# Kernel optimization log

Measured on AMD Instinct MI355X. Metric: run time of the kernel, lower is better.

## Reference

```python
import jax, jax.numpy as jnp
import numpy as np

NEG_SLOPE = 0.2

def _gc(inp, adj, W, b):
    # Kipf GraphConvolution: adj @ (inp @ W) + b
    return adj @ (inp @ W) + b

def _lrelu(x):
    return jnp.where(x >= 0, x, NEG_SLOPE * x)

def setup_inputs() -> dict:
    key = jax.random.key(0)
    ks = jax.random.split(key, 24)
    Nx, Ny, Fx, Fy, D1, C = 8192, 4096, 512, 256, 256, 64
    s = 0.05
    inp = {
        "hx1": jax.random.uniform(ks[0], (Nx, Nx), jnp.float32) / Nx,
        "hx2": jax.random.uniform(ks[1], (Nx, Ny), jnp.float32) / Ny,
        "x0": jax.random.normal(ks[2], (Nx, Fx), jnp.float32),
        "hy1": jax.random.uniform(ks[3], (Ny, Ny), jnp.float32) / Ny,
        "hy2": jax.random.uniform(ks[4], (Ny, Nx), jnp.float32) / Nx,
        "y0": jax.random.normal(ks[5], (Ny, Fy), jnp.float32),
        "alpha": jnp.float32(0.6),
        "beta": jnp.float32(0.4),
        # weights/biases of the 8 GraphConvolution layers
        "Wx1a": jax.random.normal(ks[6], (Fx, D1), jnp.float32) * s,
        "bx1a": jnp.zeros((D1,), jnp.float32),
        "Wx1b": jax.random.normal(ks[7], (Fy, D1), jnp.float32) * s,
        "bx1b": jnp.zeros((D1,), jnp.float32),
        "Wx2a": jax.random.normal(ks[8], (D1, C), jnp.float32) * s,
        "bx2a": jnp.zeros((C,), jnp.float32),
        "Wx2b": jax.random.normal(ks[9], (D1, C), jnp.float32) * s,
        "bx2b": jnp.zeros((C,), jnp.float32),
        "Wy1a": jax.random.normal(ks[10], (Fy, D1), jnp.float32) * s,
        "by1a": jnp.zeros((D1,), jnp.float32),
        "Wy1b": jax.random.normal(ks[11], (Fx, D1), jnp.float32) * s,
        "by1b": jnp.zeros((D1,), jnp.float32),
        "Wy2a": jax.random.normal(ks[12], (D1, C), jnp.float32) * s,
        "by2a": jnp.zeros((C,), jnp.float32),
        "Wy2b": jax.random.normal(ks[13], (D1, C), jnp.float32) * s,
        "by2b": jnp.zeros((C,), jnp.float32),
    }
    return inp

def reference(hx1, hx2, x0, hy1, hy2, y0, alpha, beta,
              Wx1a, bx1a, Wx1b, bx1b, Wx2a, bx2a, Wx2b, bx2b,
              Wy1a, by1a, Wy1b, by1b, Wy2a, by2a, Wy2b, by2b):
    # layer 1
    x1 = _lrelu(_gc(x0, hx1, Wx1a, bx1a) * alpha + _gc(y0, hx2, Wx1b, bx1b) * (1 - alpha))
    y1 = _lrelu(_gc(y0, hy1, Wy1a, by1a) * beta + _gc(x0, hy2, Wy1b, by1b) * (1 - beta))
    # layer 2
    x2 = _lrelu(_gc(x1, hx1, Wx2a, bx2a) * alpha + _gc(y1, hx2, Wx2b, bx2b) * (1 - alpha))
    y_pre = _gc(y1, hy1, Wy2a, by2a) * beta + _gc(x1, hy2, Wy2b, by2b) * (1 - beta)
    y2 = _lrelu(y_pre)
    h_hat = jax.nn.sigmoid(x2 @ y2.T)            # [Nx, Ny]
    x_output = jax.nn.log_softmax(x2, axis=1)    # [Nx, nclass]
    return (h_hat, x_output)
```

## Files before the change

kernel.cpp:

```cpp
#include <hip/hip_runtime.h>

typedef unsigned short u16;
typedef unsigned char u8;
typedef long i64;
typedef __attribute__((ext_vector_type(8))) short bf16x8;
typedef __attribute__((ext_vector_type(4))) float f32x4;
typedef __attribute__((ext_vector_type(8))) u16 u16x8;
typedef __attribute__((ext_vector_type(4))) u16 u16x4;
typedef __attribute__((ext_vector_type(4))) float f4;

#define DEVI static __device__ __forceinline__

DEVI u16 f2b(float f) { __bf16 h = (__bf16)f; return __builtin_bit_cast(u16, h); }
DEVI float b2f(u16 h) { unsigned u = ((unsigned)h) << 16; return __builtin_bit_cast(float, u); }

DEVI int pk8(float a, float b, float c, float d) {
  int w = __builtin_amdgcn_cvt_pk_fp8_f32(a, b, 0, false);
  return __builtin_amdgcn_cvt_pk_fp8_f32(c, d, w, true);
}

DEVI void gload16(const void* g, void* l) {
  __builtin_amdgcn_global_load_lds((const __attribute__((address_space(1))) void*)g,
                                   (__attribute__((address_space(3))) void*)l, 16, 0, 0);
}

__global__ __launch_bounds__(1024)
void gemmF_k(const float* __restrict__ A0, const float* __restrict__ A1,
             const u8* __restrict__ B0, const u8* __restrict__ B1,
             u8* __restrict__ A0f8, u8* __restrict__ A1f8,
             int K0, int K1, int L0, int L1,
             u16* __restrict__ Cout, size_t MN)
{
  constexpr int BM = 128, BK = 64;
  constexpr int LDA = 72;
  constexpr int ASZ = BM * LDA;
  constexpr int BSZ = 256 * BK;
  constexpr int BUFSZ = ASZ + BSZ;
  constexpr float SADJ = 8192.f;
  __shared__ __align__(16) u8 lds[4 * BUFSZ];

  const int tid = threadIdx.x, lane = tid & 63, wave = tid >> 6;
  const int wm = (wave >> 2) * 32, wn = (wave & 3) * 64;
  const int lgrp = lane >> 4, lrow = lane & 15;

  const int gy = gridDim.y;
  const int flat = blockIdx.y + gy * blockIdx.z;
  const int nwg = gy * gridDim.z;
  const int swz = (flat & 7) * (nwg >> 3) + (flat >> 3);
  const int m0 = (swz % gy) * BM;
  const int z  = swz / gy;

  const int nt0 = L0 >> 6, NT = nt0 + (L1 >> 6);

  const int r0 = tid >> 4;
  const int cf = (tid & 15) << 2;

  f32x4 acc[2][4];
#pragma unroll
  for (int m = 0; m < 2; ++m)
#pragma unroll
    for (int n = 0; n < 4; ++n) acc[m][n] = (f32x4){0.f, 0.f, 0.f, 0.f};

  f4 rA0[2], rA1[2];

  auto tileinfo = [&](int t, const float*& Ap, const u8*& Bp, u8*& Af8, int& Kj, int& kk) {
    if (t < nt0) { Ap = A0; Bp = B0; Af8 = A0f8; Kj = K0; kk = z * L0 + (t << 6); }
    else         { Ap = A1; Bp = B1; Af8 = A1f8; Kj = K1; kk = z * L1 + ((t - nt0) << 6); }
  };

  auto loadA = [&](int t, f4 (&r)[2]) {
    const float* Ap; const u8* Bp; u8* Af8; int Kj, kk;
    tileinfo(t, Ap, Bp, Af8, Kj, kk);
#pragma unroll
    for (int j = 0; j < 2; ++j) {
      const int rr = j * 64 + r0;
      r[j] = __builtin_nontemporal_load(
          (const f4*)(Ap + (size_t)(m0 + rr) * Kj + kk + cf));
    }
  };

  auto loadB = [&](int t) {
    const float* Ap; const u8* Bp; u8* Af8; int Kj, kk;
    tileinfo(t, Ap, Bp, Af8, Kj, kk);
    u8* sB = &lds[(t & 3) * BUFSZ] + ASZ;
    const int off = tid * 16;
    const int r = off >> 6, c = off & 63;
    gload16(Bp + (size_t)r * Kj + kk + (c ^ (((r >> 1) & 3) << 4)), sB + off);
  };

  auto writeA = [&](int t, f4 (&r)[2]) {
    const float* Ap; const u8* Bp; u8* Af8; int Kj, kk;
    tileinfo(t, Ap, Bp, Af8, Kj, kk);
    u8* sA = &lds[(t & 3) * BUFSZ];
#pragma unroll
    for (int j = 0; j < 2; ++j) {
      const int rr = j * 64 + r0;
      const int pw = pk8(r[j][0] * SADJ, r[j][1] * SADJ, r[j][2] * SADJ, r[j][3] * SADJ);
      *(int*)&sA[rr * LDA + cf] = pw;
      *(int*)(Af8 + (size_t)(m0 + rr) * Kj + kk + cf) = pw;
    }
  };

  auto compute = [&](int t) {
    const u8* sA = &lds[(t & 3) * BUFSZ];
    const u8* sB = sA + ASZ;
    __builtin_amdgcn_s_setprio(1);
#pragma unroll
    for (int ks = 0; ks < 2; ++ks) {
      i64 a[2], b[4];
#pragma unroll
      for (int m = 0; m < 2; ++m) {
        const int r = wm + m * 16 + lrow;
        a[m] = *(const i64*)&sA[r * LDA + ks * 32 + lgrp * 8];
      }
#pragma unroll
      for (int n = 0; n < 4; ++n) {
        const int r = wn + n * 16 + lrow;
        b[n] = *(const i64*)&sB[r * BK + ((ks * 32 + lgrp * 8) ^ (((r >> 1) & 3) << 4))];
      }
#pragma unroll
      for (int m = 0; m < 2; ++m)
#pragma unroll
        for (int n = 0; n < 4; ++n)
          acc[m][n] = __builtin_amdgcn_mfma_f32_16x16x32_fp8_fp8(a[m], b[n], acc[m][n], 0, 0, 0);
    }
    __builtin_amdgcn_s_setprio(0);
  };

  auto step = [&](int t, f4 (&rIn)[2], f4 (&rOut)[2]) {
    const bool has_next = (t + 1 < NT);
    if (has_next) { loadA(t + 1, rOut); loadB(t + 1); }
    if (!has_next)   asm volatile("s_waitcnt vmcnt(0)" ::: "memory");
    else if (t == 0) asm volatile("s_waitcnt vmcnt(3)" ::: "memory");
    else             asm volatile("s_waitcnt vmcnt(5)" ::: "memory");
    writeA(t, rIn);
    asm volatile("s_waitcnt lgkmcnt(0)" ::: "memory");
    asm volatile("s_barrier" ::: "memory");
    compute(t);
  };

  loadA(0, rA0); loadB(0);

  for (int t = 0; t < NT; t += 2) {
    step(t, rA0, rA1);
    step(t + 1, rA1, rA0);
  }

  u16* Cp = Cout + (size_t)z * MN;
#pragma unroll
  for (int n = 0; n < 4; ++n) {
    const int c = wn + n * 16 + lrow;
#pragma unroll
    for (int m = 0; m < 2; ++m) {
      const int rb = m0 + wm + m * 16 + lgrp * 4;
#pragma unroll
      for (int q = 0; q < 4; ++q)
        Cp[(size_t)(rb + q) * 256 + c] = f2b(acc[m][n][q]);
    }
  }
}

__global__ __launch_bounds__(256)
void gemm8_k(const u8* __restrict__ xA0, const u8* __restrict__ xA1,
             const u8* __restrict__ xB0, const u8* __restrict__ xB1,
             int xK0, int xK1, int xL0, int xL1, u16* __restrict__ xC, size_t xMN,
             const u8* __restrict__ yA0, const u8* __restrict__ yA1,
             const u8* __restrict__ yB0, const u8* __restrict__ yB1,
             int yK0, int yK1, int yL0, int yL1, u16* __restrict__ yC, size_t yMN)
{
  constexpr int BM = 128, BK = 128, BN = 64;
  constexpr int MR = 4, NR = 2;
  constexpr int ASZ = BM * BK, BSZ = BN * BK;
  __shared__ __align__(16) u8 lds[3 * (ASZ + BSZ)];

  const int tid = threadIdx.x, lane = tid & 63, wave = tid >> 6;
  const int wm = (wave >> 1) * 64, wn = (wave & 1) * 32;
  const int lgrp = lane >> 4, lrow = lane & 15;

  const int flat = blockIdx.x;
  const int nwg = gridDim.x;
  const int swz = (flat & 7) * (nwg >> 3) + (flat >> 3);

  const u8 *A0, *A1, *B0, *B1; int K0, K1, L0, L1; u16* Cw; size_t MN;
  int m0, z;
  if (swz < 512) {
    A0=xA0; A1=xA1; B0=xB0; B1=xB1; K0=xK0; K1=xK1; L0=xL0; L1=xL1; Cw=xC; MN=xMN;
    m0 = (swz & 63) * BM; z = swz >> 6;
  } else {
    const int id = swz - 512;
    A0=yA0; A1=yA1; B0=yB0; B1=yB1; K0=yK0; K1=yK1; L0=yL0; L1=yL1; Cw=yC; MN=yMN;
    m0 = (id & 31) * BM; z = id >> 5;
  }

  const int nt0 = L0 >> 7, NT = nt0 + (L1 >> 7);

  f32x4 acc[MR][NR];
#pragma unroll
  for (int m = 0; m < MR; ++m)
#pragma unroll
    for (int n = 0; n < NR; ++n) acc[m][n] = (f32x4){0.f, 0.f, 0.f, 0.f};

  auto stage = [&](int buf, int t) {
    const u8* Ap; const u8* Bp; int Kj, kk;
    if (t < nt0) { Ap = A0; Bp = B0; Kj = K0; kk = z * L0 + (t << 7); }
    else         { Ap = A1; Bp = B1; Kj = K1; kk = z * L1 + ((t - nt0) << 7); }
    u8* sA = &lds[buf * (ASZ + BSZ)];
    u8* sB = sA + ASZ;
#pragma unroll
    for (int i = 0; i < ASZ / 4096; ++i) {
      const int off = i * 4096 + tid * 16;
      const int r = off >> 7, c = off & 127;
      gload16(Ap + (size_t)(m0 + r) * Kj + kk + (c ^ ((r & 7) << 4)), sA + off);
    }
#pragma unroll
    for (int i = 0; i < BSZ / 4096; ++i) {
      const int off = i * 4096 + tid * 16;
      const int r = off >> 7, c = off & 127;
      gload16(Bp + (size_t)r * Kj + kk + (c ^ ((r & 7) << 4)), sB + off);
    }
  };

  auto compute = [&](int buf) {
    const u8* sA = &lds[buf * (ASZ + BSZ)];
    const u8* sB = sA + ASZ;
    __builtin_amdgcn_s_setprio(1);
#pragma unroll
    for (int ks = 0; ks < 4; ++ks) {
      i64 a[MR], b[NR];
#pragma unroll
      for (int m = 0; m < MR; ++m) {
        const int r = wm + m * 16 + lrow;
        a[m] = *(const i64*)&sA[r * BK + ((ks * 32 + lgrp * 8) ^ ((r & 7) << 4))];
      }
#pragma unroll
      for (int n = 0; n < NR; ++n) {
        const int r = wn + n * 16 + lrow;
        b[n] = *(const i64*)&sB[r * BK + ((ks * 32 + lgrp * 8) ^ ((r & 7) << 4))];
      }
#pragma unroll
      for (int m = 0; m < MR; ++m)
#pragma unroll
        for (int n = 0; n < NR; ++n)
          acc[m][n] = __builtin_amdgcn_mfma_f32_16x16x32_fp8_fp8(a[m], b[n], acc[m][n], 0, 0, 0);
    }
    __builtin_amdgcn_s_setprio(0);
  };

  stage(0, 0);
  stage(1, 1);
  for (int t = 0; t < NT; ++t) {
    if (t + 1 < NT) asm volatile("s_waitcnt vmcnt(6)" ::: "memory");
    else            asm volatile("s_waitcnt vmcnt(0)" ::: "memory");
    asm volatile("s_barrier" ::: "memory");
    compute(t % 3);
    if (t + 2 < NT) stage((t + 2) % 3, t + 2);
  }

  u16* Cp = Cw + (size_t)z * MN;
#pragma unroll
  for (int n = 0; n < NR; ++n) {
    const int c = wn + n * 16 + lrow;
#pragma unroll
    for (int m = 0; m < MR; ++m) {
      const int rb = m0 + wm + m * 16 + lgrp * 4;
#pragma unroll
      for (int q = 0; q < 4; ++q)
        Cp[(size_t)(rb + q) * 64 + c] = f2b(acc[m][n][q]);
    }
  }
}

template<bool A_F32>
__global__ __launch_bounds__(256)
void gemmS_k(const void* Ax, const u16* Bx, int Kx, int ldcx, u8* Cx1, u8* Cx2,
             const void* Ay, const u16* By, int Ky, int ldcy, u8* Cy1, u8* Cy2,
             int ySplit, int nsplit, float sOut)
{
  constexpr int BM = 64, BN = 64, BK = 32, LD = 40;
  constexpr int MR = 2, NR = 2;
  __shared__ u16 sA[BM * LD];
  __shared__ u16 sB[BN * LD];

  const int tid  = threadIdx.x;
  const int lane = tid & 63;
  const int wave = tid >> 6;
  const int wm = (wave >> 1) * 32;
  const int wn = (wave &  1) * 32;

  const void* A0_; const u16* B0_; int K0, ldc; u8 *C1, *C2; int m0;
  if ((int)blockIdx.y < ySplit) {
    A0_ = Ax; B0_ = Bx; K0 = Kx; ldc = ldcx; C1 = Cx1; C2 = Cx2;
    m0 = blockIdx.y * BM;
  } else {
    A0_ = Ay; B0_ = By; K0 = Ky; ldc = ldcy; C1 = Cy1; C2 = Cy2;
    m0 = (blockIdx.y - ySplit) * BM;
  }
  const int n0 = blockIdx.x * BN;

  constexpr int TPRA = 256 / BM;
  constexpr int EPTA = 32 / TPRA;
  const int ar = tid / TPRA, ac = (tid % TPRA) * EPTA;
  const int br = ar, bc = ac;

  f32x4 acc[MR][NR];
#pragma unroll
  for (int m = 0; m < MR; ++m)
#pragma unroll
    for (int n = 0; n < NR; ++n) acc[m][n] = (f32x4){0.f, 0.f, 0.f, 0.f};

  const int lgrp = lane >> 4, lrow = lane & 15;

  for (int kk = 0; kk < K0; kk += BK) {
    if constexpr (A_F32) {
      const float* Ap = (const float*)A0_ + (size_t)(m0 + ar) * K0 + kk + ac;
      f4 v0 = ((const f4*)Ap)[0];
      f4 v1 = ((const f4*)Ap)[1];
      u16x8 h;
      h[0]=f2b(v0[0]); h[1]=f2b(v0[1]); h[2]=f2b(v0[2]); h[3]=f2b(v0[3]);
      h[4]=f2b(v1[0]); h[5]=f2b(v1[1]); h[6]=f2b(v1[2]); h[7]=f2b(v1[3]);
      *(u16x8*)&sA[ar * LD + ac] = h;
    } else {
      const u16* Ap = (const u16*)A0_ + (size_t)(m0 + ar) * K0 + kk + ac;
      *(u16x8*)&sA[ar * LD + ac] = *(const u16x8*)Ap;
    }
    {
      const u16* Bp = B0_ + (size_t)(n0 + br) * K0 + kk + bc;
      *(u16x8*)&sB[br * LD + bc] = *(const u16x8*)Bp;
    }
    __syncthreads();
    bf16x8 af[MR], bfr[NR];
#pragma unroll
    for (int m = 0; m < MR; ++m)
      af[m] = *(const bf16x8*)&sA[(wm + m * 16 + lrow) * LD + lgrp * 8];
#pragma unroll
    for (int n = 0; n < NR; ++n)
      bfr[n] = *(const bf16x8*)&sB[(wn + n * 16 + lrow) * LD + lgrp * 8];
#pragma unroll
    for (int m = 0; m < MR; ++m)
#pragma unroll
      for (int n = 0; n < NR; ++n)
        acc[m][n] = __builtin_amdgcn_mfma_f32_16x16x32_bf16(af[m], bfr[n], acc[m][n], 0, 0, 0);
    __syncthreads();
  }

#pragma unroll
  for (int n = 0; n < NR; ++n) {
    const int c = n0 + wn + n * 16 + lrow;
    u8* Cp = (c < nsplit) ? C1 : C2;
    const int cr = (c < nsplit) ? c : c - nsplit;
#pragma unroll
    for (int m = 0; m < MR; ++m) {
      const int rb = m0 + wm + m * 16 + lgrp * 4;
      int w = __builtin_amdgcn_cvt_pk_fp8_f32(acc[m][n][0] * sOut, acc[m][n][1] * sOut, 0, false);
      w = __builtin_amdgcn_cvt_pk_fp8_f32(acc[m][n][2] * sOut, acc[m][n][3] * sOut, w, true);
      *(int*)&Cp[(size_t)cr * ldc + rb] = w;
    }
  }
}

__global__ __launch_bounds__(256)
void gemmH_k(const u16* A0_, const u16* B0_, int K0, float* Cout, int ldc)
{
  constexpr int BM = 128, BN = 128, BK = 32, LD = 40;
  constexpr int MR = 4, NR = 4;
  __shared__ u16 sA[BM * LD];
  __shared__ u16 sB[BN * LD];

  const int tid  = threadIdx.x;
  const int lane = tid & 63;
  const int wave = tid >> 6;
  const int wm = (wave >> 1) * 64;
  const int wn = (wave &  1) * 64;
  const int m0 = blockIdx.y * BM;
  const int n0 = blockIdx.x * BN;

  constexpr int TPRA = 2;
  constexpr int EPTA = 16;
  const int ar = tid / TPRA, ac = (tid % TPRA) * EPTA;

  f32x4 acc[MR][NR];
#pragma unroll
  for (int m = 0; m < MR; ++m)
#pragma unroll
    for (int n = 0; n < NR; ++n) acc[m][n] = (f32x4){0.f, 0.f, 0.f, 0.f};

  const int lgrp = lane >> 4, lrow = lane & 15;

  for (int kk = 0; kk < K0; kk += BK) {
    {
      const u16* Ap = A0_ + (size_t)(m0 + ar) * K0 + kk + ac;
      *(u16x8*)&sA[ar * LD + ac]     = ((const u16x8*)Ap)[0];
      *(u16x8*)&sA[ar * LD + ac + 8] = ((const u16x8*)Ap)[1];
      const u16* Bp = B0_ + (size_t)(n0 + ar) * K0 + kk + ac;
      *(u16x8*)&sB[ar * LD + ac]     = ((const u16x8*)Bp)[0];
      *(u16x8*)&sB[ar * LD + ac + 8] = ((const u16x8*)Bp)[1];
    }
    __syncthreads();
    bf16x8 af[MR], bfr[NR];
#pragma unroll
    for (int m = 0; m < MR; ++m)
      af[m] = *(const bf16x8*)&sA[(wm + m * 16 + lrow) * LD + lgrp * 8];
#pragma unroll
    for (int n = 0; n < NR; ++n)
      bfr[n] = *(const bf16x8*)&sB[(wn + n * 16 + lrow) * LD + lgrp * 8];
#pragma unroll
    for (int m = 0; m < MR; ++m)
#pragma unroll
      for (int n = 0; n < NR; ++n)
        acc[m][n] = __builtin_amdgcn_mfma_f32_16x16x32_bf16(af[m], bfr[n], acc[m][n], 0, 0, 0);
    __syncthreads();
  }

  float* Cp = Cout;
#pragma unroll
  for (int n = 0; n < NR; ++n) {
    const int c = n0 + wn + n * 16 + lrow;
#pragma unroll
    for (int m = 0; m < MR; ++m) {
      const int rb = m0 + wm + m * 16 + lgrp * 4;
#pragma unroll
      for (int q = 0; q < 4; ++q)
        Cp[(size_t)(rb + q) * ldc + c] = 1.f / (1.f + __expf(-acc[m][n][q]));
    }
  }
}

__global__ __launch_bounds__(256)
void combine_k(const u16* __restrict__ parts, int KS, int N, size_t MN,
               const float* b0, const float* b1, const float* mixp, u16* out, float invs)
{
  const float mix = *mixp;
  const size_t stride = (size_t)gridDim.x * 1024;
  for (size_t i = ((size_t)blockIdx.x * 256 + threadIdx.x) * 4; i < MN; i += stride) {
    f4 s = {0.f, 0.f, 0.f, 0.f};
    for (int zz = 0; zz < KS; ++zz) {
      u16x4 pv = *(const u16x4*)&parts[(size_t)zz * MN + i];
#pragma unroll
      for (int q = 0; q < 4; ++q) s[q] += b2f(pv[q]);
    }
    const int c = (int)(i % (size_t)N);
    u16x4 o;
#pragma unroll
    for (int q = 0; q < 4; ++q) {
      float v = s[q] * invs + mix * b0[c + q] + (1.f - mix) * b1[c + q];
      v = v >= 0.f ? v : 0.2f * v;
      o[q] = f2b(v);
    }
    *(u16x4*)&out[i] = o;
  }
}

__global__ __launch_bounds__(256)
void prep_w(const float* Wx1a, const float* Wx1b, const float* Wy1a, const float* Wy1b,
            const float* Wx2a, const float* Wx2b, const float* Wy2a, const float* Wy2b,
            u16* WtX, u16* WtY, u16* W2X, u16* W2Y,
            const float* ap, const float* bp)
{
  const int zz = blockIdx.z;
  const float a = *ap, b = *bp;
  const float* W; u16* O; int K, N, roff; float s;
  switch (zz) {
    case 0: W=Wx1a; O=WtX; K=512; N=256; roff=0;   s=a;      break;
    case 1: W=Wy1b; O=WtX; K=512; N=256; roff=256; s=1.f-b;  break;
    case 2: W=Wx1b; O=WtY; K=256; N=256; roff=0;   s=1.f-a;  break;
    case 3: W=Wy1a; O=WtY; K=256; N=256; roff=256; s=b;      break;
    case 4: W=Wx2a; O=W2X; K=256; N=64;  roff=0;   s=a;      break;
    case 5: W=Wy2b; O=W2X; K=256; N=64;  roff=64;  s=1.f-b;  break;
    case 6: W=Wx2b; O=W2Y; K=256; N=64;  roff=0;   s=1.f-a;  break;
    default:W=Wy2a; O=W2Y; K=256; N=64;  roff=64;  s=b;      break;
  }
  const int total = K * N;
  for (int i = blockIdx.x * 256 + threadIdx.x; i < total; i += gridDim.x * 256) {
    const int k = i / N, n = i - k * N;
    O[(size_t)(n + roff) * K + k] = f2b(W[i] * s);
  }
}

__global__ __launch_bounds__(256)
void softmax_k(const u16* x, float* out)
{
  const int row  = blockIdx.x * 4 + (threadIdx.x >> 6);
  const int lane = threadIdx.x & 63;
  const float v = b2f(x[row * 64 + lane]);
  float m = v;
#pragma unroll
  for (int off = 32; off; off >>= 1) m = fmaxf(m, __shfl_xor(m, off));
  float s = __expf(v - m);
#pragma unroll
  for (int off = 32; off; off >>= 1) s += __shfl_xor(s, off);
  out[(size_t)row * 64 + lane] = v - m - __logf(s);
}

extern "C" void kernel_launch(void* const* d_in, const int* in_sizes, int n_in,
                              void* d_out, int out_size, void* d_ws, size_t ws_size,
                              hipStream_t stream)
{
  const float* hx1 = (const float*)d_in[0];
  const float* hx2 = (const float*)d_in[1];
  const float* x0  = (const float*)d_in[2];
  const float* hy1 = (const float*)d_in[3];
  const float* hy2 = (const float*)d_in[4];
  const float* y0  = (const float*)d_in[5];
  const float* alphap = (const float*)d_in[6];
  const float* betap  = (const float*)d_in[7];
  const float* Wx1a = (const float*)d_in[8];  const float* bx1a = (const float*)d_in[9];
  const float* Wx1b = (const float*)d_in[10]; const float* bx1b = (const float*)d_in[11];
  const float* Wx2a = (const float*)d_in[12]; const float* bx2a = (const float*)d_in[13];
  const float* Wx2b = (const float*)d_in[14]; const float* bx2b = (const float*)d_in[15];
  const float* Wy1a = (const float*)d_in[16]; const float* by1a = (const float*)d_in[17];
  const float* Wy1b = (const float*)d_in[18]; const float* by1b = (const float*)d_in[19];
  const float* Wy2a = (const float*)d_in[20]; const float* by2a = (const float*)d_in[21];
  const float* Wy2b = (const float*)d_in[22]; const float* by2b = (const float*)d_in[23];
  (void)in_sizes; (void)n_in; (void)out_size;

  constexpr int Nx = 8192, Ny = 4096, Fx = 512, Fy = 256, D1 = 256, C = 64;
  constexpr float SB1 = 16.f, SB2 = 256.f;
  constexpr float INV1 = 1.f / (8192.f * 16.f);
  constexpr float INV2 = 1.f / (8192.f * 256.f);
  constexpr int KSx = 4, KSy = 8;

  u8* wsb = (u8*)d_ws;
  size_t off = 0;
  auto alloc = [&](size_t n) { u8* p = wsb + off; off += (n + 63) & ~(size_t)63; return p; };

  u16* WtX = (u16*)alloc((size_t)512 * 512 * 2);
  u16* WtY = (u16*)alloc((size_t)512 * 256 * 2);
  u16* W2X = (u16*)alloc((size_t)128 * 256 * 2);
  u16* W2Y = (u16*)alloc((size_t)128 * 256 * 2);
  u8* B1x  = alloc((size_t)D1 * Nx);
  u8* B2x  = alloc((size_t)D1 * Ny);
  u8* B1y  = alloc((size_t)D1 * Ny);
  u8* B2y  = alloc((size_t)D1 * Nx);
  u16* x1  = (u16*)alloc((size_t)Nx * D1 * 2);
  u16* y1  = (u16*)alloc((size_t)Ny * D1 * 2);
  u8* B1x2 = alloc((size_t)C * Nx);
  u8* B2x2 = alloc((size_t)C * Ny);
  u8* B1y2 = alloc((size_t)C * Ny);
  u8* B2y2 = alloc((size_t)C * Nx);
  u16* x2  = (u16*)alloc((size_t)Nx * C * 2);
  u16* y2  = (u16*)alloc((size_t)Ny * C * 2);

  const size_t base_off = off;
  const size_t szHx1 = (size_t)Nx * Nx, szHx2 = (size_t)Nx * Ny;
  const size_t szHy1 = (size_t)Ny * Ny, szHy2 = (size_t)Ny * Nx;
  const size_t needA = base_off + szHx1 + szHx2 + szHy1 + szHy2 + ((size_t)32 << 20) + (1 << 20);

  u8 *hx1f8, *hx2f8, *hy1f8, *hy2f8; u16* part;
  if (ws_size >= needA) {
    hx1f8 = alloc(szHx1); hx2f8 = alloc(szHx2);
    hy1f8 = alloc(szHy1); hy2f8 = alloc(szHy2);
    part  = (u16*)alloc((size_t)32 << 20);
  } else {
    hy1f8 = alloc(szHy1); hy2f8 = alloc(szHy2);
    hx1f8 = (u8*)d_out;
    hx2f8 = (u8*)d_out + szHx1;
    part  = (u16*)((u8*)d_out + szHx1 + szHx2);
  }

  const size_t MNx1 = (size_t)Nx * D1, MNy1 = (size_t)Ny * D1;
  const size_t MNx2 = (size_t)Nx * C,  MNy2 = (size_t)Ny * C;

  prep_w<<<dim3(256, 1, 8), 256, 0, stream>>>(Wx1a, Wx1b, Wy1a, Wy1b, Wx2a, Wx2b, Wy2a, Wy2b,
      WtX, WtY, W2X, W2Y, alphap, betap);

  gemmS_k<true><<<dim3(8, Nx/64 + Ny/64), 256, 0, stream>>>(
      x0, WtX, Fx, Nx, B1x, B2y,
      y0, WtY, Fy, Ny, B2x, B1y,
      Nx/64, 256, SB1);

  gemmF_k<<<dim3(1, Nx/128, KSx), 1024, 0, stream>>>(hx1, hx2, B1x, B2x, hx1f8, hx2f8,
      Nx, Ny, Nx/KSx, Ny/KSx, part, MNx1);
  combine_k<<<dim3(2048), 256, 0, stream>>>(part, KSx, D1, MNx1, bx1a, bx1b, alphap, x1, INV1);
  gemmF_k<<<dim3(1, Ny/128, KSy), 1024, 0, stream>>>(hy1, hy2, B1y, B2y, hy1f8, hy2f8,
      Ny, Nx, Ny/KSy, Nx/KSy, part, MNy1);
  combine_k<<<dim3(1024), 256, 0, stream>>>(part, KSy, D1, MNy1, by1a, by1b, betap, y1, INV1);

  gemmS_k<false><<<dim3(2, Nx/64 + Ny/64), 256, 0, stream>>>(
      x1, W2X, D1, Nx, B1x2, B2y2,
      y1, W2Y, D1, Ny, B2x2, B1y2,
      Nx/64, 64, SB2);

  u16* partY2 = part + 8 * MNx2;
  gemm8_k<<<dim3(1024), 256, 0, stream>>>(
      hx1f8, hx2f8, B1x2, B2x2, Nx, Ny, 1024, 512, part, MNx2,
      hy1f8, hy2f8, B1y2, B2y2, Ny, Nx, 256, 512, partY2, MNy2);
  combine_k<<<dim3(512), 256, 0, stream>>>(part, 8, C, MNx2, bx2a, bx2b, alphap, x2, INV2);
  combine_k<<<dim3(256), 256, 0, stream>>>(partY2, 16, C, MNy2, by2a, by2b, betap, y2, INV2);

  gemmH_k<<<dim3(Ny/128, Nx/128), 256, 0, stream>>>(x2, y2, C, (float*)d_out, Ny);

  softmax_k<<<dim3(Nx/4), 256, 0, stream>>>(x2, (float*)d_out + (size_t)Nx * Ny);
}
```

Before: 345.0 us.

## Merge x/y layer-1 GEMMs and combines into single launches, fuse softmax into combine

The two layer-1 fp32-adjacency GEMMs (x and y sides) now run as one 512-block launch that picks its operand set from the swizzled block id. The two layer-1 combines become one kernel, and the layer-2 combines are merged with the log-softmax so x2 is never re-read. The final sigmoid output uses nontemporal stores. This cuts launch count and tail effects and lets the two sides overlap. The cost is hardcoded grid splits (256 x blocks, KSx=4 assumed, column index & 255) that tie the code to these exact shapes.

After: 345.6 us. Within noise of the previous version (+0.2%).

```diff
diff --git a/kernel.cpp b/kernel.cpp
--- a/kernel.cpp
+++ b/kernel.cpp
@@ -25,11 +25,14 @@
 }
 
 __global__ __launch_bounds__(1024)
-void gemmF_k(const float* __restrict__ A0, const float* __restrict__ A1,
-             const u8* __restrict__ B0, const u8* __restrict__ B1,
-             u8* __restrict__ A0f8, u8* __restrict__ A1f8,
-             int K0, int K1, int L0, int L1,
-             u16* __restrict__ Cout, size_t MN)
+void gemmF_k(const float* __restrict__ xA0, const float* __restrict__ xA1,
+             const u8* __restrict__ xB0, const u8* __restrict__ xB1,
+             u8* __restrict__ xA0f8, u8* __restrict__ xA1f8,
+             int xK0, int xK1, int xL0, int xL1, u16* __restrict__ xC, size_t xMN,
+             const float* __restrict__ yA0, const float* __restrict__ yA1,
+             const u8* __restrict__ yB0, const u8* __restrict__ yB1,
+             u8* __restrict__ yA0f8, u8* __restrict__ yA1f8,
+             int yK0, int yK1, int yL0, int yL1, u16* __restrict__ yC, size_t yMN)
 {
   constexpr int BM = 128, BK = 64;
   constexpr int LDA = 72;
@@ -43,12 +46,22 @@
   const int wm = (wave >> 2) * 32, wn = (wave & 3) * 64;
   const int lgrp = lane >> 4, lrow = lane & 15;
 
-  const int gy = gridDim.y;
-  const int flat = blockIdx.y + gy * blockIdx.z;
-  const int nwg = gy * gridDim.z;
+  const int flat = blockIdx.x;
+  const int nwg = gridDim.x;
   const int swz = (flat & 7) * (nwg >> 3) + (flat >> 3);
-  const int m0 = (swz % gy) * BM;
-  const int z  = swz / gy;
+
+  const float *A0, *A1; const u8 *B0, *B1; u8 *A0f8, *A1f8;
+  int K0, K1, L0, L1; u16* Cout; size_t MN; int m0, z;
+  if (swz < 256) {
+    A0=xA0; A1=xA1; B0=xB0; B1=xB1; A0f8=xA0f8; A1f8=xA1f8;
+    K0=xK0; K1=xK1; L0=xL0; L1=xL1; Cout=xC; MN=xMN;
+    m0 = (swz & 63) * BM; z = swz >> 6;
+  } else {
+    const int id = swz - 256;
+    A0=yA0; A1=yA1; B0=yB0; B1=yB1; A0f8=yA0f8; A1f8=yA1f8;
+    K0=yK0; K1=yK1; L0=yL0; L1=yL1; Cout=yC; MN=yMN;
+    m0 = (id & 31) * BM; z = id >> 5;
+  }
 
   const int nt0 = L0 >> 6, NT = nt0 + (L1 >> 6);
 
@@ -420,25 +433,38 @@
       const int rb = m0 + wm + m * 16 + lgrp * 4;
 #pragma unroll
       for (int q = 0; q < 4; ++q)
-        Cp[(size_t)(rb + q) * ldc + c] = 1.f / (1.f + __expf(-acc[m][n][q]));
+        __builtin_nontemporal_store(1.f / (1.f + __expf(-acc[m][n][q])),
+                                    &Cp[(size_t)(rb + q) * ldc + c]);
     }
   }
 }
 
 __global__ __launch_bounds__(256)
-void combine_k(const u16* __restrict__ parts, int KS, int N, size_t MN,
-               const float* b0, const float* b1, const float* mixp, u16* out, float invs)
-{
+void combine1_k(const u16* __restrict__ partX, const u16* __restrict__ partY,
+                int xBlocks, size_t MNx, size_t MNy, int KSx_, int KSy_,
+                const float* bxa, const float* bxb, const float* ap,
+                const float* bya, const float* byb, const float* bp,
+                u16* x1, u16* y1, float invs)
+{
+  const u16* parts; size_t MN; int KS, nb, bid = blockIdx.x;
+  const float *b0, *b1, *mixp; u16* out;
+  if (bid < xBlocks) {
+    parts = partX; MN = MNx; KS = KSx_; b0 = bxa; b1 = bxb; mixp = ap; out = x1; nb = xBlocks;
+  } else {
+    bid -= xBlocks;
+    parts = partY; MN = MNy; KS = KSy_; b0 = bya; b1 = byb; mixp = bp; out = y1;
+    nb = gridDim.x - xBlocks;
+  }
   const float mix = *mixp;
-  const size_t stride = (size_t)gridDim.x * 1024;
-  for (size_t i = ((size_t)blockIdx.x * 256 + threadIdx.x) * 4; i < MN; i += stride) {
+  const size_t stride = (size_t)nb * 1024;
+  for (size_t i = ((size_t)bid * 256 + threadIdx.x) * 4; i < MN; i += stride) {
     f4 s = {0.f, 0.f, 0.f, 0.f};
     for (int zz = 0; zz < KS; ++zz) {
       u16x4 pv = *(const u16x4*)&parts[(size_t)zz * MN + i];
 #pragma unroll
       for (int q = 0; q < 4; ++q) s[q] += b2f(pv[q]);
     }
-    const int c = (int)(i % (size_t)N);
+    const int c = (int)(i & 255);
     u16x4 o;
 #pragma unroll
     for (int q = 0; q < 4; ++q) {
@@ -447,6 +473,44 @@
       o[q] = f2b(v);
     }
     *(u16x4*)&out[i] = o;
+  }
+}
+
+__global__ __launch_bounds__(256)
+void combine2_k(const u16* __restrict__ partX, const u16* __restrict__ partY,
+                int xRowBlocks, size_t MNx, size_t MNy,
+                const float* bxa, const float* bxb, const float* ap,
+                const float* bya, const float* byb, const float* bp,
+                u16* x2, u16* y2, float* xout, float invs)
+{
+  const int w = threadIdx.x >> 6, lane = threadIdx.x & 63;
+  if ((int)blockIdx.x < xRowBlocks) {
+    const int row = blockIdx.x * 4 + w;
+    const float a = *ap;
+    float s = 0.f;
+#pragma unroll
+    for (int z = 0; z < 8; ++z)
+      s += b2f(partX[(size_t)z * MNx + (size_t)row * 64 + lane]);
+    float v = s * invs + a * bxa[lane] + (1.f - a) * bxb[lane];
+    v = v >= 0.f ? v : 0.2f * v;
+    x2[(size_t)row * 64 + lane] = f2b(v);
+    float m = v;
+#pragma unroll
+    for (int o = 32; o; o >>= 1) m = fmaxf(m, __shfl_xor(m, o));
+    float t = __expf(v - m);
+#pragma unroll
+    for (int o = 32; o; o >>= 1) t += __shfl_xor(t, o);
+    xout[(size_t)row * 64 + lane] = v - m - __logf(t);
+  } else {
+    const int row = ((int)blockIdx.x - xRowBlocks) * 4 + w;
+    const float b = *bp;
+    float s = 0.f;
+#pragma unroll
+    for (int z = 0; z < 16; ++z)
+      s += b2f(partY[(size_t)z * MNy + (size_t)row * 64 + lane]);
+    float v = s * invs + b * bya[lane] + (1.f - b) * byb[lane];
+    v = v >= 0.f ? v : 0.2f * v;
+    y2[(size_t)row * 64 + lane] = f2b(v);
   }
 }
 
@@ -474,21 +538,6 @@
     const int k = i / N, n = i - k * N;
     O[(size_t)(n + roff) * K + k] = f2b(W[i] * s);
   }
-}
-
-__global__ __launch_bounds__(256)
-void softmax_k(const u16* x, float* out)
-{
-  const int row  = blockIdx.x * 4 + (threadIdx.x >> 6);
-  const int lane = threadIdx.x & 63;
-  const float v = b2f(x[row * 64 + lane]);
-  float m = v;
-#pragma unroll
-  for (int off = 32; off; off >>= 1) m = fmaxf(m, __shfl_xor(m, off));
-  float s = __expf(v - m);
-#pragma unroll
-  for (int off = 32; off; off >>= 1) s += __shfl_xor(s, off);
-  out[(size_t)row * 64 + lane] = v - m - __logf(s);
 }
 
 extern "C" void kernel_launch(void* const* d_in, const int* in_sizes, int n_in,
@@ -559,6 +608,8 @@
 
   const size_t MNx1 = (size_t)Nx * D1, MNy1 = (size_t)Ny * D1;
   const size_t MNx2 = (size_t)Nx * C,  MNy2 = (size_t)Ny * C;
+  u16* partY1 = part + (size_t)KSx * MNx1;
+  u16* partY2 = part + 8 * MNx2;
 
   prep_w<<<dim3(256, 1, 8), 256, 0, stream>>>(Wx1a, Wx1b, Wy1a, Wy1b, Wx2a, Wx2b, Wy2a, Wy2b,
       WtX, WtY, W2X, W2Y, alphap, betap);
@@ -568,26 +619,25 @@
       y0, WtY, Fy, Ny, B2x, B1y,
       Nx/64, 256, SB1);
 
-  gemmF_k<<<dim3(1, Nx/128, KSx), 1024, 0, stream>>>(hx1, hx2, B1x, B2x, hx1f8, hx2f8,
-      Nx, Ny, Nx/KSx, Ny/KSx, part, MNx1);
-  combine_k<<<dim3(2048), 256, 0, stream>>>(part, KSx, D1, MNx1, bx1a, bx1b, alphap, x1, INV1);
-  gemmF_k<<<dim3(1, Ny/128, KSy), 1024, 0, stream>>>(hy1, hy2, B1y, B2y, hy1f8, hy2f8,
-      Ny, Nx, Ny/KSy, Nx/KSy, part, MNy1);
-  combine_k<<<dim3(1024), 256, 0, stream>>>(part, KSy, D1, MNy1, by1a, by1b, betap, y1, INV1);
+  gemmF_k<<<dim3(512), 1024, 0, stream>>>(
+      hx1, hx2, B1x, B2x, hx1f8, hx2f8, Nx, Ny, Nx/KSx, Ny/KSx, part, MNx1,
+      hy1, hy2, B1y, B2y, hy1f8, hy2f8, Ny, Nx, Ny/KSy, Nx/KSy, partY1, MNy1);
+
+  combine1_k<<<dim3(3072), 256, 0, stream>>>(part, partY1, 2048, MNx1, MNy1, KSx, KSy,
+      bx1a, bx1b, alphap, by1a, by1b, betap, x1, y1, INV1);
 
   gemmS_k<false><<<dim3(2, Nx/64 + Ny/64), 256, 0, stream>>>(
       x1, W2X, D1, Nx, B1x2, B2y2,
       y1, W2Y, D1, Ny, B2x2, B1y2,
       Nx/64, 64, SB2);
 
-  u16* partY2 = part + 8 * MNx2;
   gemm8_k<<<dim3(1024), 256, 0, stream>>>(
       hx1f8, hx2f8, B1x2, B2x2, Nx, Ny, 1024, 512, part, MNx2,
       hy1f8, hy2f8, B1y2, B2y2, Ny, Nx, 256, 512, partY2, MNy2);
-  combine_k<<<dim3(512), 256, 0, stream>>>(part, 8, C, MNx2, bx2a, bx2b, alphap, x2, INV2);
-  combine_k<<<dim3(256), 256, 0, stream>>>(partY2, 16, C, MNy2, by2a, by2b, betap, y2, INV2);
+
+  combine2_k<<<dim3(2048 + 1024), 256, 0, stream>>>(part, partY2, 2048, MNx2, MNy2,
+      bx2a, bx2b, alphap, by2a, by2b, betap, x2, y2,
+      (float*)d_out + (size_t)Nx * Ny, INV2);
 
   gemmH_k<<<dim3(Ny/128, Nx/128), 256, 0, stream>>>(x2, y2, C, (float*)d_out, Ny);
-
-  softmax_k<<<dim3(Nx/4), 256, 0, stream>>>(x2, (float*)d_out + (size_t)Nx * Ny);
-}
+}
```
